# Performance work log

Hardware: AMD Instinct MI355X
Metric: run time of the kernel (lower is better)

Reference implementation:

```python
import jax, jax.numpy as jnp
import numpy as np

N_NODE = 8192
H1 = 512
R_EMB = 128
N_EDGE = 262144
N_REG = 2048


def gcn_conv(x, W, b, src, dst, n):
    """PyG-style GCNConv: add self-loops, sym-normalize, linear, scatter-add."""
    h = x @ W  # [n, out]
    loop = jnp.arange(n)
    src2 = jnp.concatenate([src, loop])
    dst2 = jnp.concatenate([dst, loop])
    ones = jnp.ones(src2.shape[0], dtype=h.dtype)
    deg = jax.ops.segment_sum(ones, dst2, num_segments=n)  # in-degree incl. self-loop
    dis = jnp.where(deg > 0, jax.lax.rsqrt(deg), 0.0)
    norm = dis[src2] * dis[dst2]  # [E+n]
    msg = h[src2] * norm[:, None]  # gather + scale
    return jax.ops.segment_sum(msg, dst2, num_segments=n) + b


def setup_inputs() -> dict:
    key = jax.random.key(0)
    k1, k2, k3, k4 = jax.random.split(key, 4)
    edge_index = jax.random.randint(k1, (N_EDGE, 2), 0, N_NODE)  # [E,2] (src,dst) pairs
    reg_id = jax.random.randint(k2, (N_REG,), 0, N_NODE)
    W1 = jax.random.normal(k3, (N_NODE, H1), dtype=jnp.float32) * 0.02
    b1 = jnp.zeros((H1,), dtype=jnp.float32)
    W2 = jax.random.normal(k4, (H1, R_EMB), dtype=jnp.float32) * 0.02
    b2 = jnp.zeros((R_EMB,), dtype=jnp.float32)
    return {"reg_id": reg_id, "edge_index": edge_index, "W1": W1, "b1": b1, "W2": W2, "b2": b2}


def reference(reg_id, edge_index, W1, b1, W2, b2):
    src = edge_index[:, 0]
    dst = edge_index[:, 1]
    n = W1.shape[0]
    x = jnp.eye(n, dtype=W1.dtype)  # identity feature matrix (one-hot per node)
    h = jax.nn.relu(gcn_conv(x, W1, b1, src, dst, n))
    # dropout is identity at inference
    out = gcn_conv(h, W2, b2, src, dst, n)  # [n, R_EMB]
    return out[reg_id]
```

## Files before the change

kernel.cpp:

```cpp
#include <hip/hip_runtime.h>
#include <hip/hip_bf16.h>

typedef unsigned int u32;

#define N_NODE 8192
#define H1 512
#define R_EMB 128
#define N_EDGE 262144
#define N_REG 2048

#define OFF_DEG        (0)
#define OFF_ROWSTART   (64 * 1024)
#define OFF_CURSOR     (128 * 1024)
#define OFF_DIS        (160 * 1024)
#define OFF_SORTED     (256 * 1024)
#define OFF_W1S        (2 * 1024 * 1024)
#define OFF_H1S        (10 * 1024 * 1024)
#define OFF_W2T        (18 * 1024 * 1024)
#define OFF_G          (19 * 1024 * 1024)

__device__ inline u32 rne_bf16(float f) {
    u32 u = __float_as_uint(f);
    u += 0x7fffu + ((u >> 16) & 1u);
    return u >> 16;
}
__device__ inline float bf_lo(u32 u) { return __uint_as_float(u << 16); }
__device__ inline float bf_hi(u32 u) { return __uint_as_float(u & 0xffff0000u); }

using frag_ab = __attribute__((ext_vector_type(8))) short;
using frag_cd = __attribute__((ext_vector_type(4))) float;

__global__ void hist_kernel(const int* __restrict__ edge, int* __restrict__ deg) {
    int e = blockIdx.x * blockDim.x + threadIdx.x;
    if (e < N_EDGE) {
        int dst = edge[2 * e + 1];
        atomicAdd(&deg[dst], 1);
    }
}

__global__ void scan_kernel(const int* __restrict__ deg, int* __restrict__ row_start,
                            int* __restrict__ cursor, float* __restrict__ dis) {
    __shared__ int part[1024];
    int t = threadIdx.x;
    int base = t * 8;
    int local[8];
    int sum = 0;
#pragma unroll
    for (int j = 0; j < 8; j++) {
        local[j] = deg[base + j];
        sum += local[j];
    }
    part[t] = sum;
    __syncthreads();
    for (int off = 1; off < 1024; off <<= 1) {
        int v = part[t];
        int add = (t >= off) ? part[t - off] : 0;
        __syncthreads();
        part[t] = v + add;
        __syncthreads();
    }
    int run = part[t] - sum;
#pragma unroll
    for (int j = 0; j < 8; j++) {
        row_start[base + j] = run;
        cursor[base + j] = run;
        dis[base + j] = rsqrtf((float)(local[j] + 1));
        run += local[j];
    }
    if (t == 1023) row_start[N_NODE] = run;
}

__global__ void fill_kernel(const int* __restrict__ edge, int* __restrict__ cursor,
                            int* __restrict__ sorted_src) {
    int e = blockIdx.x * blockDim.x + threadIdx.x;
    if (e < N_EDGE) {
        int src = edge[2 * e + 0];
        int dst = edge[2 * e + 1];
        int pos = atomicAdd(&cursor[dst], 1);
        sorted_src[pos] = src;
    }
}

__global__ void convert_kernel(const float* __restrict__ W1, const float* __restrict__ dis,
                               u32* __restrict__ W1s) {
    int idx = blockIdx.x * blockDim.x + threadIdx.x;
    int row = idx >> 8;
    int pc = idx & 255;
    float d = dis[row];
    float2 f = *(const float2*)(W1 + ((size_t)row << 9) + (pc << 1));
    W1s[idx] = rne_bf16(f.x * d) | (rne_bf16(f.y * d) << 16);
}

__global__ void convert_w2t_kernel(const float* __restrict__ W2, u32* __restrict__ w2t) {
    int idx = blockIdx.x * blockDim.x + threadIdx.x;
    int j = idx >> 8;
    int p = idx & 255;
    float a = W2[(size_t)(2 * p) * R_EMB + j];
    float b = W2[(size_t)(2 * p + 1) * R_EMB + j];
    w2t[idx] = rne_bf16(a) | (rne_bf16(b) << 16);
}

__global__ void layer1_kernel(const u32* __restrict__ W1s, const float* __restrict__ b1,
                              const int* __restrict__ row_start, const int* __restrict__ sorted_src,
                              const float* __restrict__ dis, u32* __restrict__ h1s) {
    int d = blockIdx.x;
    int t = threadIdx.x;
    float disd = dis[d];
    const uint4* base = (const uint4*)W1s;

    uint4 w = base[(d << 6) + t];
    float a0 = bf_lo(w.x), a1 = bf_hi(w.x), a2 = bf_lo(w.y), a3 = bf_hi(w.y);
    float a4 = bf_lo(w.z), a5 = bf_hi(w.z), a6 = bf_lo(w.w), a7 = bf_hi(w.w);

    int beg = row_start[d], end = row_start[d + 1];
    for (int i = beg; i < end; i++) {
        int s = sorted_src[i];
        uint4 ws = base[(s << 6) + t];
        a0 += bf_lo(ws.x); a1 += bf_hi(ws.x);
        a2 += bf_lo(ws.y); a3 += bf_hi(ws.y);
        a4 += bf_lo(ws.z); a5 += bf_hi(ws.z);
        a6 += bf_lo(ws.w); a7 += bf_hi(ws.w);
    }
    int f = t * 8;
    float4 bl = *(const float4*)(b1 + f);
    float4 bh = *(const float4*)(b1 + f + 4);
    float o0 = fmaxf(a0 * disd + bl.x, 0.0f) * disd;
    float o1 = fmaxf(a1 * disd + bl.y, 0.0f) * disd;
    float o2 = fmaxf(a2 * disd + bl.z, 0.0f) * disd;
    float o3 = fmaxf(a3 * disd + bl.w, 0.0f) * disd;
    float o4 = fmaxf(a4 * disd + bh.x, 0.0f) * disd;
    float o5 = fmaxf(a5 * disd + bh.y, 0.0f) * disd;
    float o6 = fmaxf(a6 * disd + bh.z, 0.0f) * disd;
    float o7 = fmaxf(a7 * disd + bh.w, 0.0f) * disd;
    uint4 o;
    o.x = rne_bf16(o0) | (rne_bf16(o1) << 16);
    o.y = rne_bf16(o2) | (rne_bf16(o3) << 16);
    o.z = rne_bf16(o4) | (rne_bf16(o5) << 16);
    o.w = rne_bf16(o6) | (rne_bf16(o7) << 16);
    ((uint4*)h1s)[(d << 6) + t] = o;
}

__global__ void layer2_agg_kernel(const u32* __restrict__ h1s, const int* __restrict__ reg_id,
                                  const int* __restrict__ row_start, const int* __restrict__ sorted_src,
                                  const float* __restrict__ dis, u32* __restrict__ g_bf) {
    int tgt = blockIdx.x;
    int d = reg_id[tgt];
    int t = threadIdx.x;
    float disd = dis[d];
    const uint4* base = (const uint4*)h1s;

    uint4 w = base[(d << 6) + t];
    float a0 = bf_lo(w.x), a1 = bf_hi(w.x), a2 = bf_lo(w.y), a3 = bf_hi(w.y);
    float a4 = bf_lo(w.z), a5 = bf_hi(w.z), a6 = bf_lo(w.w), a7 = bf_hi(w.w);

    int beg = row_start[d], end = row_start[d + 1];
    for (int i = beg; i < end; i++) {
        int s = sorted_src[i];
        uint4 ws = base[(s << 6) + t];
        a0 += bf_lo(ws.x); a1 += bf_hi(ws.x);
        a2 += bf_lo(ws.y); a3 += bf_hi(ws.y);
        a4 += bf_lo(ws.z); a5 += bf_hi(ws.z);
        a6 += bf_lo(ws.w); a7 += bf_hi(ws.w);
    }
    uint4 o;
    o.x = rne_bf16(a0 * disd) | (rne_bf16(a1 * disd) << 16);
    o.y = rne_bf16(a2 * disd) | (rne_bf16(a3 * disd) << 16);
    o.z = rne_bf16(a4 * disd) | (rne_bf16(a5 * disd) << 16);
    o.w = rne_bf16(a6 * disd) | (rne_bf16(a7 * disd) << 16);
    ((uint4*)g_bf)[(tgt << 6) + t] = o;
}

__global__ void gemm_out_mfma(const u32* __restrict__ g_bf, const u32* __restrict__ w2t_bf,
                              const float* __restrict__ b2, float* __restrict__ out) {
    int w = blockIdx.x * 4 + (threadIdx.x >> 6);
    int lane = threadIdx.x & 63;
    int tm = w >> 3;
    int tn = w & 7;
    int r15 = lane & 15;
    int kb4 = (lane >> 4) << 2;

    const uint4* arow = (const uint4*)(g_bf + ((tm * 16 + r15) << 8) + kb4);
    const uint4* brow = (const uint4*)(w2t_bf + ((tn * 16 + r15) << 8) + kb4);
    frag_cd acc = {0.0f, 0.0f, 0.0f, 0.0f};
#pragma unroll
    for (int kk = 0; kk < 16; kk++) {
        uint4 av = arow[kk * 4];
        uint4 bv = brow[kk * 4];
        acc = __builtin_amdgcn_mfma_f32_16x16x32_bf16(*(frag_ab*)&av, *(frag_ab*)&bv, acc, 0, 0, 0);
    }
    int col = tn * 16 + r15;
    int row0 = tm * 16 + ((lane >> 4) << 2);
    float bias = b2[col];
#pragma unroll
    for (int r = 0; r < 4; r++)
        out[(size_t)(row0 + r) * R_EMB + col] = acc[r] + bias;
}

extern "C" void kernel_launch(void* const* d_in, const int* in_sizes, int n_in,
                              void* d_out, int out_size, void* d_ws, size_t ws_size,
                              hipStream_t stream) {
    const int* reg_id = (const int*)d_in[0];
    const int* edge = (const int*)d_in[1];
    const float* W1 = (const float*)d_in[2];
    const float* b1 = (const float*)d_in[3];
    const float* W2 = (const float*)d_in[4];
    const float* b2 = (const float*)d_in[5];
    float* out = (float*)d_out;

    char* ws = (char*)d_ws;
    int* deg = (int*)(ws + OFF_DEG);
    int* row_start = (int*)(ws + OFF_ROWSTART);
    int* cursor = (int*)(ws + OFF_CURSOR);
    float* dis = (float*)(ws + OFF_DIS);
    int* sorted_src = (int*)(ws + OFF_SORTED);
    u32* W1s = (u32*)(ws + OFF_W1S);
    u32* h1s = (u32*)(ws + OFF_H1S);
    u32* w2t = (u32*)(ws + OFF_W2T);
    u32* g_bf = (u32*)(ws + OFF_G);

    hipMemsetAsync(deg, 0, N_NODE * sizeof(int), stream);

    hist_kernel<<<N_EDGE / 256, 256, 0, stream>>>(edge, deg);
    scan_kernel<<<1, 1024, 0, stream>>>(deg, row_start, cursor, dis);
    convert_kernel<<<(N_NODE * 256) / 256, 256, 0, stream>>>(W1, dis, W1s);
    convert_w2t_kernel<<<(N_REG * 16) / 256, 256, 0, stream>>>(W2, w2t);
    fill_kernel<<<N_EDGE / 256, 256, 0, stream>>>(edge, cursor, sorted_src);
    layer1_kernel<<<N_NODE, 64, 0, stream>>>(W1s, b1, row_start, sorted_src, dis, h1s);
    layer2_agg_kernel<<<N_REG, 64, 0, stream>>>(h1s, reg_id, row_start, sorted_src, dis, g_bf);
    gemm_out_mfma<<<256, 256, 0, stream>>>(g_bf, w2t, b2, out);
}
```

Before: 163.4 us.

## Merge prep kernels, use wave-shuffle scan, unroll gather loops by two

Three independent changes. The fill, W1-convert and W2-transpose kernels become one launch that dispatches on block index, which removes two kernel launches and their gaps. The block scan now uses wavefront shuffles plus a small cross-wave pass instead of a 1024-entry shared-memory Hillis-Steele scan with barriers at every step. The layer1 and layer2 gather loops are unrolled by two with dual accumulators so two row loads are in flight per iteration, at the cost of extra registers and a slightly different summation order.

```diff
diff --git a/kernel.cpp b/kernel.cpp
--- a/kernel.cpp
+++ b/kernel.cpp
@@ -40,8 +40,11 @@
 
 __global__ void scan_kernel(const int* __restrict__ deg, int* __restrict__ row_start,
                             int* __restrict__ cursor, float* __restrict__ dis) {
-    __shared__ int part[1024];
+    __shared__ int wtot[16];
+    __shared__ int wpre[16];
     int t = threadIdx.x;
+    int lane = t & 63;
+    int wv = t >> 6;
     int base = t * 8;
     int local[8];
     int sum = 0;
@@ -50,16 +53,26 @@
         local[j] = deg[base + j];
         sum += local[j];
     }
-    part[t] = sum;
+    int sc = sum;
+#pragma unroll
+    for (int off = 1; off < 64; off <<= 1) {
+        int y = __shfl_up(sc, off, 64);
+        if (lane >= off) sc += y;
+    }
+    if (lane == 63) wtot[wv] = sc;
     __syncthreads();
-    for (int off = 1; off < 1024; off <<= 1) {
-        int v = part[t];
-        int add = (t >= off) ? part[t - off] : 0;
-        __syncthreads();
-        part[t] = v + add;
-        __syncthreads();
-    }
-    int run = part[t] - sum;
+    if (wv == 0 && lane < 16) {
+        int v = wtot[lane];
+        int s2 = v;
+#pragma unroll
+        for (int off = 1; off < 16; off <<= 1) {
+            int y = __shfl_up(s2, off, 64);
+            if (lane >= off) s2 += y;
+        }
+        wpre[lane] = s2 - v;
+    }
+    __syncthreads();
+    int run = wpre[wv] + (sc - sum);
 #pragma unroll
     for (int j = 0; j < 8; j++) {
         row_start[base + j] = run;
@@ -70,34 +83,33 @@
     if (t == 1023) row_start[N_NODE] = run;
 }
 
-__global__ void fill_kernel(const int* __restrict__ edge, int* __restrict__ cursor,
-                            int* __restrict__ sorted_src) {
-    int e = blockIdx.x * blockDim.x + threadIdx.x;
-    if (e < N_EDGE) {
+__global__ void prep_kernel(const int* __restrict__ edge, int* __restrict__ cursor,
+                            int* __restrict__ sorted_src,
+                            const float* __restrict__ W1, const float* __restrict__ dis,
+                            u32* __restrict__ W1s,
+                            const float* __restrict__ W2, u32* __restrict__ w2t) {
+    int bid = blockIdx.x;
+    if (bid < 1024) {
+        int e = bid * 256 + threadIdx.x;
         int src = edge[2 * e + 0];
         int dst = edge[2 * e + 1];
         int pos = atomicAdd(&cursor[dst], 1);
         sorted_src[pos] = src;
-    }
-}
-
-__global__ void convert_kernel(const float* __restrict__ W1, const float* __restrict__ dis,
-                               u32* __restrict__ W1s) {
-    int idx = blockIdx.x * blockDim.x + threadIdx.x;
-    int row = idx >> 8;
-    int pc = idx & 255;
-    float d = dis[row];
-    float2 f = *(const float2*)(W1 + ((size_t)row << 9) + (pc << 1));
-    W1s[idx] = rne_bf16(f.x * d) | (rne_bf16(f.y * d) << 16);
-}
-
-__global__ void convert_w2t_kernel(const float* __restrict__ W2, u32* __restrict__ w2t) {
-    int idx = blockIdx.x * blockDim.x + threadIdx.x;
-    int j = idx >> 8;
-    int p = idx & 255;
-    float a = W2[(size_t)(2 * p) * R_EMB + j];
-    float b = W2[(size_t)(2 * p + 1) * R_EMB + j];
-    w2t[idx] = rne_bf16(a) | (rne_bf16(b) << 16);
+    } else if (bid < 1024 + 8192) {
+        int idx = (bid - 1024) * 256 + threadIdx.x;
+        int row = idx >> 8;
+        int pc = idx & 255;
+        float d = dis[row];
+        float2 f = *(const float2*)(W1 + ((size_t)row << 9) + (pc << 1));
+        W1s[idx] = rne_bf16(f.x * d) | (rne_bf16(f.y * d) << 16);
+    } else {
+        int idx = (bid - 9216) * 256 + threadIdx.x;
+        int j = idx >> 8;
+        int p = idx & 255;
+        float a = W2[(size_t)(2 * p) * R_EMB + j];
+        float b = W2[(size_t)(2 * p + 1) * R_EMB + j];
+        w2t[idx] = rne_bf16(a) | (rne_bf16(b) << 16);
+    }
 }
 
 __global__ void layer1_kernel(const u32* __restrict__ W1s, const float* __restrict__ b1,
@@ -111,16 +123,35 @@
     uint4 w = base[(d << 6) + t];
     float a0 = bf_lo(w.x), a1 = bf_hi(w.x), a2 = bf_lo(w.y), a3 = bf_hi(w.y);
     float a4 = bf_lo(w.z), a5 = bf_hi(w.z), a6 = bf_lo(w.w), a7 = bf_hi(w.w);
+    float c0 = 0, c1 = 0, c2 = 0, c3 = 0, c4 = 0, c5 = 0, c6 = 0, c7 = 0;
 
     int beg = row_start[d], end = row_start[d + 1];
-    for (int i = beg; i < end; i++) {
-        int s = sorted_src[i];
+    int i = beg;
+    if ((end - beg) & 1) {
+        int s = sorted_src[i++];
         uint4 ws = base[(s << 6) + t];
         a0 += bf_lo(ws.x); a1 += bf_hi(ws.x);
         a2 += bf_lo(ws.y); a3 += bf_hi(ws.y);
         a4 += bf_lo(ws.z); a5 += bf_hi(ws.z);
         a6 += bf_lo(ws.w); a7 += bf_hi(ws.w);
     }
+    for (; i < end; i += 2) {
+        int s0 = sorted_src[i];
+        int s1 = sorted_src[i + 1];
+        uint4 w0 = base[(s0 << 6) + t];
+        uint4 w1 = base[(s1 << 6) + t];
+        a0 += bf_lo(w0.x); a1 += bf_hi(w0.x);
+        a2 += bf_lo(w0.y); a3 += bf_hi(w0.y);
+        a4 += bf_lo(w0.z); a5 += bf_hi(w0.z);
+        a6 += bf_lo(w0.w); a7 += bf_hi(w0.w);
+        c0 += bf_lo(w1.x); c1 += bf_hi(w1.x);
+        c2 += bf_lo(w1.y); c3 += bf_hi(w1.y);
+        c4 += bf_lo(w1.z); c5 += bf_hi(w1.z);
+        c6 += bf_lo(w1.w); c7 += bf_hi(w1.w);
+    }
+    a0 += c0; a1 += c1; a2 += c2; a3 += c3;
+    a4 += c4; a5 += c5; a6 += c6; a7 += c7;
+
     int f = t * 8;
     float4 bl = *(const float4*)(b1 + f);
     float4 bh = *(const float4*)(b1 + f + 4);
@@ -152,16 +183,35 @@
     uint4 w = base[(d << 6) + t];
     float a0 = bf_lo(w.x), a1 = bf_hi(w.x), a2 = bf_lo(w.y), a3 = bf_hi(w.y);
     float a4 = bf_lo(w.z), a5 = bf_hi(w.z), a6 = bf_lo(w.w), a7 = bf_hi(w.w);
+    float c0 = 0, c1 = 0, c2 = 0, c3 = 0, c4 = 0, c5 = 0, c6 = 0, c7 = 0;
 
     int beg = row_start[d], end = row_start[d + 1];
-    for (int i = beg; i < end; i++) {
-        int s = sorted_src[i];
+    int i = beg;
+    if ((end - beg) & 1) {
+        int s = sorted_src[i++];
         uint4 ws = base[(s << 6) + t];
         a0 += bf_lo(ws.x); a1 += bf_hi(ws.x);
         a2 += bf_lo(ws.y); a3 += bf_hi(ws.y);
         a4 += bf_lo(ws.z); a5 += bf_hi(ws.z);
         a6 += bf_lo(ws.w); a7 += bf_hi(ws.w);
     }
+    for (; i < end; i += 2) {
+        int s0 = sorted_src[i];
+        int s1 = sorted_src[i + 1];
+        uint4 w0 = base[(s0 << 6) + t];
+        uint4 w1 = base[(s1 << 6) + t];
+        a0 += bf_lo(w0.x); a1 += bf_hi(w0.x);
+        a2 += bf_lo(w0.y); a3 += bf_hi(w0.y);
+        a4 += bf_lo(w0.z); a5 += bf_hi(w0.z);
+        a6 += bf_lo(w0.w); a7 += bf_hi(w0.w);
+        c0 += bf_lo(w1.x); c1 += bf_hi(w1.x);
+        c2 += bf_lo(w1.y); c3 += bf_hi(w1.y);
+        c4 += bf_lo(w1.z); c5 += bf_hi(w1.z);
+        c6 += bf_lo(w1.w); c7 += bf_hi(w1.w);
+    }
+    a0 += c0; a1 += c1; a2 += c2; a3 += c3;
+    a4 += c4; a5 += c5; a6 += c6; a7 += c7;
+
     uint4 o;
     o.x = rne_bf16(a0 * disd) | (rne_bf16(a1 * disd) << 16);
     o.y = rne_bf16(a2 * disd) | (rne_bf16(a3 * disd) << 16);
@@ -222,9 +272,8 @@
 
     hist_kernel<<<N_EDGE / 256, 256, 0, stream>>>(edge, deg);
     scan_kernel<<<1, 1024, 0, stream>>>(deg, row_start, cursor, dis);
-    convert_kernel<<<(N_NODE * 256) / 256, 256, 0, stream>>>(W1, dis, W1s);
-    convert_w2t_kernel<<<(N_REG * 16) / 256, 256, 0, stream>>>(W2, w2t);
-    fill_kernel<<<N_EDGE / 256, 256, 0, stream>>>(edge, cursor, sorted_src);
+    prep_kernel<<<1024 + 8192 + 128, 256, 0, stream>>>(edge, cursor, sorted_src,
+                                                       W1, dis, W1s, W2, w2t);
     layer1_kernel<<<N_NODE, 64, 0, stream>>>(W1s, b1, row_start, sorted_src, dis, h1s);
     layer2_agg_kernel<<<N_REG, 64, 0, stream>>>(h1s, reg_id, row_start, sorted_src, dis, g_bf);
     gemm_out_mfma<<<256, 256, 0, stream>>>(g_bf, w2t, b2, out);
```

Result: faster. 149.7 us (-8.4%).
